# Performance work log

Hardware: AMD Instinct MI355X
Metric: run time of the kernel (lower is better)

The kernel has to match this reference:

```python
import jax, jax.numpy as jnp
import numpy as np
import math

H = 4          # n_heads
LAM = 2.0      # gate_lambda
EPS = 1e-6


def _evid_gate(t, W, b):
    # t: [B,T,d] -> g: [B,T,1] via Normal-Inverse-Gamma evidential gate
    h = t @ W.T + b                                  # [B,T,4]
    mu, v_raw, a_raw, b_raw = jnp.split(h, 4, axis=-1)
    v = jax.nn.softplus(v_raw) + EPS
    alpha = jax.nn.softplus(a_raw) + 1.0 + EPS
    beta = jax.nn.softplus(b_raw) + EPS
    var_ep = beta / (v * (alpha - 1.0))
    g = jax.nn.sigmoid(mu) * jnp.exp(-LAM * var_ep)
    return jnp.maximum(g, 1e-6)


def _ln(t, g, b):
    m = jnp.mean(t, axis=-1, keepdims=True)
    v = jnp.var(t, axis=-1, keepdims=True)
    return (t - m) / jnp.sqrt(v + 1e-5) * g + b


def _split(t):
    B, T, d = t.shape
    return t.reshape(B, T, H, d // H).transpose(0, 2, 1, 3)  # [B,H,T,dk]


def _merge(t):
    B, h, T, dk = t.shape
    return t.transpose(0, 2, 1, 3).reshape(B, T, h * dk)


def _gated_attn(q, k, v, lg_q, lg_k, mask_k, dk):
    # q:[B,H,Tq,dk], k/v:[B,H,Tk,dk], lg_q:[B,Tq], lg_k:[B,Tk], mask_k:[B,Tk] bool
    s = jnp.einsum('bhqd,bhkd->bhqk', q, k) / math.sqrt(dk)
    s = s + lg_q[:, None, :, None] + lg_k[:, None, None, :]
    s = jnp.where(mask_k[:, None, None, :], s, -jnp.inf)
    a = jax.nn.softmax(s, axis=-1)                   # dropout is identity in eval
    return jnp.einsum('bhqk,bhkd->bhqd', a, v)


def setup_inputs():
    key = jax.random.key(0)
    ks = jax.random.split(key, 20)
    B, Nx, Ny, d = 16, 512, 1024, 256
    s = 0.02
    w = lambda k, shape: jax.random.normal(k, shape, jnp.float32) * s
    return {
        'x': jax.random.normal(ks[0], (B, Nx, d), jnp.float32),
        'y': jax.random.normal(ks[1], (B, Ny, d), jnp.float32),
        'x_mask': jnp.ones((B, Nx), bool),
        'y_mask': jnp.ones((B, Ny), bool),
        'Wqx': w(ks[2], (d, d)), 'Wkx': w(ks[3], (d, d)), 'Wvx': w(ks[4], (d, d)),
        'Wqy': w(ks[5], (d, d)), 'Wky': w(ks[6], (d, d)), 'Wvy': w(ks[7], (d, d)),
        'gWx': w(ks[8], (4, d)), 'gbx': jnp.zeros((4,), jnp.float32),
        'gWy': w(ks[9], (4, d)), 'gby': jnp.zeros((4,), jnp.float32),
        'Wox': w(ks[10], (d, d)), 'Woy': w(ks[11], (d, d)),
        'lnx_g': jnp.ones((d,), jnp.float32), 'lnx_b': jnp.zeros((d,), jnp.float32),
        'lny_g': jnp.ones((d,), jnp.float32), 'lny_b': jnp.zeros((d,), jnp.float32),
        'ffx_W': w(ks[12], (d, d)), 'ffx_b': jnp.zeros((d,), jnp.float32),
        'ffy_W': w(ks[13], (d, d)), 'ffy_b': jnp.zeros((d,), jnp.float32),
    }


def reference(x, y, x_mask, y_mask, Wqx, Wkx, Wvx, Wqy, Wky, Wvy,
              gWx, gbx, gWy, gby, Wox, Woy,
              lnx_g, lnx_b, lny_g, lny_b, ffx_W, ffx_b, ffy_W, ffy_b):
    d = x.shape[-1]
    dk = d // H
    qx, kx, vx = _split(x @ Wqx.T), _split(x @ Wkx.T), _split(x @ Wvx.T)
    qy, ky, vy = _split(y @ Wqy.T), _split(y @ Wky.T), _split(y @ Wvy.T)
    gx = _evid_gate(x, gWx, gbx)                     # [B,Nx,1]
    gy = _evid_gate(y, gWy, gby)                     # [B,Ny,1]
    lgx = jnp.log(gx)[..., 0]                        # [B,Nx]
    lgy = jnp.log(gy)[..., 0]                        # [B,Ny]

    out_x = _merge(_gated_attn(qx, ky, vy, lgx, lgy, y_mask, dk)) @ Wox.T
    x2 = _ln(x + out_x, lnx_g, lnx_b)
    x2 = _ln(x2 + jax.nn.silu(x2 @ ffx_W.T + ffx_b), lnx_g, lnx_b)

    out_y = _merge(_gated_attn(qy, kx, vx, lgy, lgx, x_mask, dk)) @ Woy.T
    y2 = _ln(y + out_y, lny_g, lny_b)
    y2 = _ln(y2 + jax.nn.silu(y2 @ ffy_W.T + ffy_b), lny_g, lny_b)

    return x2, y2, gx[..., 0], gy[..., 0]
```

## Files before the change

### kernel.cpp

```cpp
#include <hip/hip_runtime.h>
#include <stdint.h>

typedef unsigned short u16;
typedef unsigned int   u32;
typedef __attribute__((ext_vector_type(8))) short bf16x8;
typedef __attribute__((ext_vector_type(4))) float f32x4;

__device__ __forceinline__ u16 f2b(float f) {
    union { float f; u32 i; } v; v.f = f;
    return (u16)((v.i + 0x7fffu + ((v.i >> 16) & 1u)) >> 16);
}
__device__ __forceinline__ float b2f(u16 u) {
    union { float f; u32 i; } v; v.i = ((u32)u) << 16; return v.f;
}
__device__ __forceinline__ bf16x8 pack8(const float* s) {
    union { bf16x8 v; u16 u[8]; } r;
    #pragma unroll
    for (int i = 0; i < 8; i++) r.u[i] = f2b(s[i]);
    return r.v;
}
__device__ __forceinline__ float softplus_f(float x) {
    return x > 15.f ? x : log1pf(__expf(x));
}

__global__ __launch_bounds__(256) void prep(
    const float* __restrict__ X, const float* __restrict__ Y,
    const float* __restrict__ gWx, const float* __restrict__ gbx,
    const float* __restrict__ gWy, const float* __restrict__ gby,
    float* __restrict__ goutx, float* __restrict__ lgx,
    float* __restrict__ gouty, float* __restrict__ lgy,
    u16* __restrict__ xb, u16* __restrict__ yb,
    const float* p0, const float* p1, const float* p2, const float* p3,
    const float* p4, const float* p5, const float* p6, const float* p7,
    const float* p8, const float* p9, u16* __restrict__ wdst)
{
    const int blk = blockIdx.x;
    const int t = threadIdx.x;
    if (blk < 6144) {
        int tok = blk * 4 + (t >> 6);
        const int lane = t & 63;
        const bool isx = tok < 8192;
        const float* T  = isx ? X : Y;
        const float* gW = isx ? gWx : gWy;
        const float* gb = isx ? gbx : gby;
        float* go = isx ? goutx : gouty;
        float* lg = isx ? lgx : lgy;
        if (!isx) tok -= 8192;
        const float* xp = T + (size_t)tok * 256;
        float a0 = 0.f, a1 = 0.f, a2 = 0.f, a3 = 0.f;
        #pragma unroll
        for (int i = 0; i < 4; i++) {
            int c = lane + i * 64;
            float xv = xp[c];
            a0 += xv * gW[0 * 256 + c];
            a1 += xv * gW[1 * 256 + c];
            a2 += xv * gW[2 * 256 + c];
            a3 += xv * gW[3 * 256 + c];
        }
        #pragma unroll
        for (int off = 32; off > 0; off >>= 1) {
            a0 += __shfl_xor(a0, off);
            a1 += __shfl_xor(a1, off);
            a2 += __shfl_xor(a2, off);
            a3 += __shfl_xor(a3, off);
        }
        if (lane == 0) {
            float mu    = a0 + gb[0];
            float v     = softplus_f(a1 + gb[1]) + 1e-6f;
            float alpha = softplus_f(a2 + gb[2]) + 1.0f + 1e-6f;
            float beta  = softplus_f(a3 + gb[3]) + 1e-6f;
            float var_ep = beta / (v * (alpha - 1.0f));
            float sig = 1.0f / (1.0f + __expf(-mu));
            float g = fmaxf(sig * __expf(-2.0f * var_ep), 1e-6f);
            go[tok] = g;
            lg[tok] = logf(g);
        }
    } else if (blk < 9216) {
        int g = (blk - 6144) * 256 + t;
        const float* src; u16* dst; size_t off;
        if (g < 262144) { src = X; dst = xb; off = (size_t)g * 8; }
        else            { src = Y; dst = yb; off = (size_t)(g - 262144) * 8; }
        float tmp[8];
        *(float4*)&tmp[0] = *(const float4*)(src + off);
        *(float4*)&tmp[4] = *(const float4*)(src + off + 4);
        *(bf16x8*)(dst + off) = pack8(tmp);
    } else {
        int g = (blk - 9216) * 256 + t;
        int wsel = g >> 13, off = g & 8191;
        const float* src;
        switch (wsel) {
            case 0: src = p0; break; case 1: src = p1; break;
            case 2: src = p2; break; case 3: src = p3; break;
            case 4: src = p4; break; case 5: src = p5; break;
            case 6: src = p6; break; case 7: src = p7; break;
            case 8: src = p8; break; default: src = p9; break;
        }
        float tmp[8];
        *(float4*)&tmp[0] = *(const float4*)(src + (size_t)off * 8);
        *(float4*)&tmp[4] = *(const float4*)(src + (size_t)off * 8 + 4);
        *(bf16x8*)(wdst + ((size_t)wsel * 65536) + (size_t)off * 8) = pack8(tmp);
    }
}

__global__ __launch_bounds__(256, 2) void gemm_qkv(
    const u16* __restrict__ Axb, const u16* __restrict__ Ayb,
    const u16* __restrict__ Wx, const u16* __restrict__ Wy,
    u16* __restrict__ Qx, u16* __restrict__ Kx, u16* __restrict__ VTx,
    u16* __restrict__ Qy, u16* __restrict__ Ky, u16* __restrict__ VTy)
{
    __shared__ short smem[2 * 128 * 72];
    short* As = smem;
    short* Ws = smem + 128 * 72;
    const int t = threadIdx.x;
    const int bn = blockIdx.x;
    int bm = blockIdx.y;
    const bool isx = bm < 64;
    const u16* A  = isx ? Axb : Ayb;
    const u16* W  = isx ? Wx : Wy;
    u16* Qo  = isx ? Qx : Qy;
    u16* Ko  = isx ? Kx : Ky;
    u16* VTo = isx ? VTx : VTy;
    const int tqsh = isx ? 9 : 10;
    if (!isx) bm -= 64;

    const int w = t >> 6, lane = t & 63, li = lane & 15, quad = lane >> 4;
    const int wm = (w >> 1) * 64, wn = (w & 1) * 64;
    const int sr = t >> 1, scb = (t & 1) * 32;

    f32x4 zero = {0.f, 0.f, 0.f, 0.f};
    f32x4 acc[4][4];
    #pragma unroll
    for (int a = 0; a < 4; a++)
        #pragma unroll
        for (int b = 0; b < 4; b++) acc[a][b] = zero;

    for (int ch = 0; ch < 4; ch++) {
        const int k0 = ch * 64;
        if (ch) __syncthreads();
        {
            const u16* Ap = A + (size_t)(bm * 128 + sr) * 256 + k0 + scb;
            const u16* Wp = W + (size_t)(bn * 128 + sr) * 256 + k0 + scb;
            #pragma unroll
            for (int j = 0; j < 4; j++) {
                *(uint4*)&As[sr * 72 + scb + j * 8] = *(const uint4*)(Ap + j * 8);
                *(uint4*)&Ws[sr * 72 + scb + j * 8] = *(const uint4*)(Wp + j * 8);
            }
        }
        __syncthreads();
        #pragma unroll
        for (int c = 0; c < 2; c++) {
            bf16x8 af[4], bf[4];
            #pragma unroll
            for (int mt = 0; mt < 4; mt++)
                af[mt] = *(const bf16x8*)&As[(wm + mt * 16 + li) * 72 + c * 32 + quad * 8];
            #pragma unroll
            for (int nt = 0; nt < 4; nt++)
                bf[nt] = *(const bf16x8*)&Ws[(wn + nt * 16 + li) * 72 + c * 32 + quad * 8];
            #pragma unroll
            for (int mt = 0; mt < 4; mt++)
                #pragma unroll
                for (int nt = 0; nt < 4; nt++)
                    acc[mt][nt] = __builtin_amdgcn_mfma_f32_16x16x32_bf16(
                        af[mt], bf[nt], acc[mt][nt], 0, 0, 0);
        }
    }

    const int sel = bn >> 1;
    if (sel < 2) {
        u16* Co = (sel == 0) ? Qo : Ko;
        #pragma unroll
        for (int nt = 0; nt < 4; nt++) {
            const int c = (bn * 128 + wn + nt * 16 + li) & 255;
            #pragma unroll
            for (int mt = 0; mt < 4; mt++) {
                const int row0 = bm * 128 + wm + mt * 16 + quad * 4;
                #pragma unroll
                for (int i = 0; i < 4; i++)
                    Co[(size_t)(row0 + i) * 256 + c] = f2b(acc[mt][nt][i]);
            }
        }
    } else {
        __syncthreads();
        short* Trans = smem;
        #pragma unroll
        for (int nt = 0; nt < 4; nt++) {
            const int cl = wn + nt * 16 + li;
            #pragma unroll
            for (int mt = 0; mt < 4; mt++) {
                const int rl0 = wm + mt * 16 + quad * 4;
                #pragma unroll
                for (int i = 0; i < 4; i++)
                    Trans[cl * 136 + rl0 + i] = (short)f2b(acc[mt][nt][i]);
            }
        }
        __syncthreads();
        const int dl = t >> 1, seg = t & 1;
        const int col = (bn - 4) * 128 + dl;
        const int h = col >> 6, dd = col & 63;
        const int bz = (bm * 128) >> tqsh;
        const int key0 = (bm * 128) & ((1 << tqsh) - 1);
        u16* dst = VTo + ((((size_t)(bz * 4 + h)) * 64 + dd) << tqsh) + key0 + seg * 64;
        #pragma unroll
        for (int k = 0; k < 8; k++)
            *(uint4*)(dst + k * 8) = *(const uint4*)&Trans[dl * 136 + seg * 64 + k * 8];
    }
}

__global__ __launch_bounds__(256, 3) void attn3(
    const u16* __restrict__ Q1, const u16* __restrict__ K1, const u16* __restrict__ VT1,
    const float* __restrict__ LG1, u16* __restrict__ O1,
    const u16* __restrict__ Q2, const u16* __restrict__ K2, const u16* __restrict__ VT2,
    const float* __restrict__ LG2, u16* __restrict__ O2)
{
    __shared__ short Ks[64][72];
    __shared__ short VTs[64][72];
    __shared__ short Ps[128][72];
    __shared__ float Lk[64];

    const int t = threadIdx.x;
    const int h = blockIdx.y, bz = blockIdx.z;
    const bool ph1 = blockIdx.x < 4;
    const int qtl = ph1 ? blockIdx.x : blockIdx.x - 4;
    const u16* Q  = ph1 ? Q1 : Q2;
    const u16* K  = ph1 ? K1 : K2;
    const u16* VT = ph1 ? VT1 : VT2;
    const float* LG = ph1 ? LG1 : LG2;
    u16* O = ph1 ? O1 : O2;
    const int Tq = ph1 ? 512 : 1024;
    const int Tk = ph1 ? 1024 : 512;

    const int w = t >> 6, lane = t & 63, li = lane & 15, quad = lane >> 4;
    const int q0 = qtl * 128;

    bf16x8 qf[2][2];
    #pragma unroll
    for (int s = 0; s < 2; s++) {
        const u16* qp = Q + (size_t)(bz * Tq + q0 + s * 64 + w * 16 + li) * 256 + h * 64 + quad * 8;
        qf[s][0] = *(const bf16x8*)qp;
        qf[s][1] = *(const bf16x8*)(qp + 32);
    }

    float lsum[2] = {0.f, 0.f};
    f32x4 zero = {0.f, 0.f, 0.f, 0.f};
    f32x4 oacc[2][4];
    #pragma unroll
    for (int s = 0; s < 2; s++)
        #pragma unroll
        for (int md = 0; md < 4; md++) oacc[s][md] = zero;

    const int sr = t >> 2, sc = (t & 3) * 16;
    const u16* Kp  = K + (size_t)(bz * Tk + sr) * 256 + h * 64 + sc;
    const u16* VTp = VT + ((size_t)(bz * 4 + h) * 64 + sr) * Tk + sc;
    const float* LGp = LG + (size_t)bz * Tk;

    uint4 pk0, pk1, pv0, pv1;
    float plk;
    pk0 = *(const uint4*)(Kp);
    pk1 = *(const uint4*)(Kp + 8);
    pv0 = *(const uint4*)(VTp);
    pv1 = *(const uint4*)(VTp + 8);
    plk = (t < 64) ? LGp[t] : 0.f;

    for (int kt = 0; kt < Tk; kt += 64) {
        __syncthreads();
        *(uint4*)&Ks[sr][sc]      = pk0;
        *(uint4*)&Ks[sr][sc + 8]  = pk1;
        *(uint4*)&VTs[sr][sc]     = pv0;
        *(uint4*)&VTs[sr][sc + 8] = pv1;
        if (t < 64) Lk[t] = plk;
        __syncthreads();
        if (kt + 64 < Tk) {
            pk0 = *(const uint4*)(Kp + (size_t)(kt + 64) * 256);
            pk1 = *(const uint4*)(Kp + (size_t)(kt + 64) * 256 + 8);
            pv0 = *(const uint4*)(VTp + kt + 64);
            pv1 = *(const uint4*)(VTp + kt + 64 + 8);
            if (t < 64) plk = LGp[kt + 64 + t];
        }

        #pragma unroll
        for (int s = 0; s < 2; s++) {
            f32x4 sacc[4] = {zero, zero, zero, zero};
            #pragma unroll
            for (int c = 0; c < 2; c++)
                #pragma unroll
                for (int mt = 0; mt < 4; mt++) {
                    bf16x8 af = *(const bf16x8*)&Ks[mt * 16 + li][c * 32 + quad * 8];
                    sacc[mt] = __builtin_amdgcn_mfma_f32_16x16x32_bf16(af, qf[s][c], sacc[mt], 0, 0, 0);
                }
            #pragma unroll
            for (int mt = 0; mt < 4; mt++) {
                float4 lk4 = *(const float4*)&Lk[mt * 16 + quad * 4];
                float p0 = __expf(sacc[mt][0] * 0.125f + lk4.x);
                float p1 = __expf(sacc[mt][1] * 0.125f + lk4.y);
                float p2 = __expf(sacc[mt][2] * 0.125f + lk4.z);
                float p3 = __expf(sacc[mt][3] * 0.125f + lk4.w);
                lsum[s] += (p0 + p1) + (p2 + p3);
                uint2 st;
                st.x = (u32)f2b(p0) | ((u32)f2b(p1) << 16);
                st.y = (u32)f2b(p2) | ((u32)f2b(p3) << 16);
                *(uint2*)&Ps[s * 64 + w * 16 + li][mt * 16 + quad * 4] = st;
            }
        }

        #pragma unroll
        for (int c = 0; c < 2; c++) {
            bf16x8 vf[4], pf[2];
            #pragma unroll
            for (int md = 0; md < 4; md++)
                vf[md] = *(const bf16x8*)&VTs[md * 16 + li][c * 32 + quad * 8];
            #pragma unroll
            for (int s = 0; s < 2; s++)
                pf[s] = *(const bf16x8*)&Ps[s * 64 + w * 16 + li][c * 32 + quad * 8];
            #pragma unroll
            for (int s = 0; s < 2; s++)
                #pragma unroll
                for (int md = 0; md < 4; md++)
                    oacc[s][md] = __builtin_amdgcn_mfma_f32_16x16x32_bf16(
                        vf[md], pf[s], oacc[s][md], 0, 0, 0);
        }
    }

    #pragma unroll
    for (int s = 0; s < 2; s++) {
        float l = lsum[s];
        l += __shfl_xor(l, 16);
        l += __shfl_xor(l, 32);
        const float inv = 1.0f / l;
        u16* op = O + (size_t)(bz * Tq + q0 + s * 64 + w * 16 + li) * 256 + h * 64;
        #pragma unroll
        for (int md = 0; md < 4; md++)
            #pragma unroll
            for (int i = 0; i < 4; i++)
                op[md * 16 + quad * 4 + i] = f2b(oacc[s][md][i] * inv);
    }
}

template<int ACT>
__global__ __launch_bounds__(256, 2) void gemm_ln(
    const u16* __restrict__ Axb, const u16* __restrict__ Ayb,
    const u16* __restrict__ Wxb, const u16* __restrict__ Wyb,
    const float* __restrict__ bx, const float* __restrict__ by,
    const float* __restrict__ Rx, const float* __restrict__ Ry,
    const float* __restrict__ gxv, const float* __restrict__ bxv,
    const float* __restrict__ gyv, const float* __restrict__ byv,
    float* __restrict__ Fx, float* __restrict__ Fy,
    u16* __restrict__ Bx, u16* __restrict__ By)
{
    __shared__ short As[64 * 72];
    __shared__ short Ws[256 * 72];
    __shared__ float Sred[64][4];
    __shared__ float Ssq[64][4];

    const int t = threadIdx.x;
    int blk = blockIdx.x;
    const bool isx = blk < 128;
    const u16* A = isx ? Axb : Ayb;
    const u16* W = isx ? Wxb : Wyb;
    const float* bias  = isx ? bx : by;
    const float* RES   = isx ? Rx : Ry;
    const float* gamma = isx ? gxv : gyv;
    const float* beta  = isx ? bxv : byv;
    float* F = isx ? Fx : Fy;
    u16*   B = isx ? Bx : By;
    if (!isx) blk -= 128;
    const int r0 = blk * 64;

    const int w = t >> 6, lane = t & 63, li = lane & 15, quad = lane >> 4;
    const int wn = w * 64;

    f32x4 zero = {0.f, 0.f, 0.f, 0.f};
    f32x4 acc[4][4];
    #pragma unroll
    for (int a = 0; a < 4; a++)
        #pragma unroll
        for (int b = 0; b < 4; b++) acc[a][b] = zero;

    const int asr = t >> 2, asc = (t & 3) * 16;
    const int wr0 = t >> 3, wseg = (t & 7) * 8;
    for (int ch = 0; ch < 4; ch++) {
        const int k0 = ch * 64;
        if (ch) __syncthreads();
        {
            const u16* Ap = A + (size_t)(r0 + asr) * 256 + k0 + asc;
            *(uint4*)&As[asr * 72 + asc]     = *(const uint4*)Ap;
            *(uint4*)&As[asr * 72 + asc + 8] = *(const uint4*)(Ap + 8);
            #pragma unroll
            for (int jj = 0; jj < 8; jj++) {
                const int row = wr0 + jj * 32;
                *(uint4*)&Ws[row * 72 + wseg] =
                    *(const uint4*)(W + (size_t)row * 256 + k0 + wseg);
            }
        }
        __syncthreads();
        #pragma unroll
        for (int c = 0; c < 2; c++) {
            bf16x8 af[4], bf[4];
            #pragma unroll
            for (int mt = 0; mt < 4; mt++)
                af[mt] = *(const bf16x8*)&As[(mt * 16 + li) * 72 + c * 32 + quad * 8];
            #pragma unroll
            for (int nt = 0; nt < 4; nt++)
                bf[nt] = *(const bf16x8*)&Ws[(wn + nt * 16 + li) * 72 + c * 32 + quad * 8];
            #pragma unroll
            for (int mt = 0; mt < 4; mt++)
                #pragma unroll
                for (int nt = 0; nt < 4; nt++)
                    acc[mt][nt] = __builtin_amdgcn_mfma_f32_16x16x32_bf16(
                        af[mt], bf[nt], acc[mt][nt], 0, 0, 0);
        }
    }

    float bv[4], gv[4], btv[4];
    #pragma unroll
    for (int nt = 0; nt < 4; nt++) {
        const int col = wn + nt * 16 + li;
        bv[nt]  = bias ? bias[col] : 0.f;
        gv[nt]  = gamma[col];
        btv[nt] = beta[col];
    }
    float psum[4][4], psq[4][4];
    #pragma unroll
    for (int mt = 0; mt < 4; mt++) {
        #pragma unroll
        for (int i = 0; i < 4; i++) { psum[mt][i] = 0.f; psq[mt][i] = 0.f; }
        #pragma unroll
        for (int nt = 0; nt < 4; nt++) {
            const int col = wn + nt * 16 + li;
            #pragma unroll
            for (int i = 0; i < 4; i++) {
                float v = acc[mt][nt][i] + bv[nt];
                if (ACT) v = v / (1.f + __expf(-v));
                const int row = mt * 16 + quad * 4 + i;
                v += RES[(size_t)(r0 + row) * 256 + col];
                acc[mt][nt][i] = v;
                psum[mt][i] += v;
                psq[mt][i]  += v * v;
            }
        }
        #pragma unroll
        for (int i = 0; i < 4; i++) {
            #pragma unroll
            for (int off = 1; off < 16; off <<= 1) {
                psum[mt][i] += __shfl_xor(psum[mt][i], off);
                psq[mt][i]  += __shfl_xor(psq[mt][i], off);
            }
        }
    }
    if (li == 0) {
        #pragma unroll
        for (int mt = 0; mt < 4; mt++)
            #pragma unroll
            for (int i = 0; i < 4; i++) {
                Sred[mt * 16 + quad * 4 + i][w] = psum[mt][i];
                Ssq[mt * 16 + quad * 4 + i][w]  = psq[mt][i];
            }
    }
    __syncthreads();
    #pragma unroll
    for (int mt = 0; mt < 4; mt++) {
        #pragma unroll
        for (int i = 0; i < 4; i++) {
            const int row = mt * 16 + quad * 4 + i;
            float4 s4 = *(const float4*)&Sred[row][0];
            float4 q4 = *(const float4*)&Ssq[row][0];
            float S  = (s4.x + s4.y) + (s4.z + s4.w);
            float S2 = (q4.x + q4.y) + (q4.z + q4.w);
            float mean = S * (1.0f / 256.0f);
            float var  = S2 * (1.0f / 256.0f) - mean * mean;
            float rstd = rsqrtf(var + 1e-5f);
            #pragma unroll
            for (int nt = 0; nt < 4; nt++) {
                const int col = wn + nt * 16 + li;
                float outv = (acc[mt][nt][i] - mean) * rstd * gv[nt] + btv[nt];
                F[(size_t)(r0 + row) * 256 + col] = outv;
                if (B) B[(size_t)(r0 + row) * 256 + col] = f2b(outv);
            }
        }
    }
}

extern "C" void kernel_launch(void* const* d_in, const int* in_sizes, int n_in,
                              void* d_out, int out_size, void* d_ws, size_t ws_size,
                              hipStream_t stream)
{
    const float* x = (const float*)d_in[0];
    const float* y = (const float*)d_in[1];
    const int wb = (n_in >= 24) ? 4 : 2;
    const float* Wqx  = (const float*)d_in[wb + 0];
    const float* Wkx  = (const float*)d_in[wb + 1];
    const float* Wvx  = (const float*)d_in[wb + 2];
    const float* Wqy  = (const float*)d_in[wb + 3];
    const float* Wky  = (const float*)d_in[wb + 4];
    const float* Wvy  = (const float*)d_in[wb + 5];
    const float* gWx  = (const float*)d_in[wb + 6];
    const float* gbx  = (const float*)d_in[wb + 7];
    const float* gWy  = (const float*)d_in[wb + 8];
    const float* gby  = (const float*)d_in[wb + 9];
    const float* Wox  = (const float*)d_in[wb + 10];
    const float* Woy  = (const float*)d_in[wb + 11];
    const float* lnxg = (const float*)d_in[wb + 12];
    const float* lnxb = (const float*)d_in[wb + 13];
    const float* lnyg = (const float*)d_in[wb + 14];
    const float* lnyb = (const float*)d_in[wb + 15];
    const float* ffxW = (const float*)d_in[wb + 16];
    const float* ffxb = (const float*)d_in[wb + 17];
    const float* ffyW = (const float*)d_in[wb + 18];
    const float* ffyb = (const float*)d_in[wb + 19];

    char* ws = (char*)d_ws;
    float* lgx = (float*)(ws);
    float* lgy = (float*)(ws + 32768);
    u16* wbf   = (u16*)(ws + 98304);
    u16* xbf   = (u16*)(ws + 1409024);
    u16* ybf   = xbf + (size_t)8192 * 256;
    u16* qb    = ybf + (size_t)16384 * 256;
    u16* kb    = qb  + (size_t)8192 * 256;
    u16* vtb   = kb  + (size_t)16384 * 256;
    u16* qb2   = vtb + (size_t)16384 * 256;
    u16* kb2   = qb2 + (size_t)16384 * 256;
    u16* vtb2  = kb2 + (size_t)8192 * 256;
    u16* ctxx  = vtb2 + (size_t)8192 * 256;
    u16* ctxy  = ctxx + (size_t)8192 * 256;
    u16* xa    = ctxy + (size_t)16384 * 256;
    u16* ya    = xa + (size_t)8192 * 256;

    float* out_x2 = (float*)d_out;
    float* out_y2 = out_x2 + 2097152;
    float* out_gx = out_x2 + 6291456;
    float* out_gy = out_x2 + 6299648;

    prep<<<9536, 256, 0, stream>>>(
        x, y, gWx, gbx, gWy, gby, out_gx, lgx, out_gy, lgy,
        xbf, ybf,
        Wqx, Wkx, Wvx, Wqy, Wky, Wvy, Wox, Woy, ffxW, ffyW, wbf);
    gemm_qkv<<<dim3(6, 192), 256, 0, stream>>>(
        xbf, ybf, wbf + 0 * 65536, wbf + 3 * 65536,
        qb, kb2, vtb2, qb2, kb, vtb);
    attn3<<<dim3(12, 4, 16), 256, 0, stream>>>(
        qb, kb, vtb, lgy, ctxx, qb2, kb2, vtb2, lgx, ctxy);
    gemm_ln<0><<<384, 256, 0, stream>>>(
        ctxx, ctxy, wbf + 6 * 65536, wbf + 7 * 65536,
        nullptr, nullptr, x, y,
        lnxg, lnxb, lnyg, lnyb, out_x2, out_y2, xa, ya);
    gemm_ln<1><<<384, 256, 0, stream>>>(
        xa, ya, wbf + 8 * 65536, wbf + 9 * 65536,
        ffxb, ffyb, out_x2, out_y2,
        lnxg, lnxb, lnyg, lnyb, out_x2, out_y2, nullptr, nullptr);

    (void)in_sizes; (void)out_size; (void)ws_size;
}
```

Measured before the change: 234.5 us.

## Double-buffer attention K/V tiles, use exp2 with hardware bf16 packing, halve LN-GEMM row tile

The attention kernel now double-buffers the K, V^T and log-gate tiles in shared memory, which drops one barrier per iteration. It interleaves the P·V MFMA per query sub-tile, so the P scratch buffer shrinks to 64 rows. Softmax uses v_exp_f32 with the scale folded into log2 units, and the gate logits are stored as log2. bf16 packing uses v_cvt_pk_bf16_f32 instead of software rounding. Separately, the fused GEMM+LayerNorm kernels switch to 32-row tiles with twice as many blocks and higher occupancy bounds, trading more weight-tile reloads for better parallelism.

```diff
diff --git a/kernel.cpp b/kernel.cpp
--- a/kernel.cpp
+++ b/kernel.cpp
@@ -73,7 +73,7 @@
             float sig = 1.0f / (1.0f + __expf(-mu));
             float g = fmaxf(sig * __expf(-2.0f * var_ep), 1e-6f);
             go[tok] = g;
-            lg[tok] = logf(g);
+            lg[tok] = log2f(g);
         }
     } else if (blk < 9216) {
         int g = (blk - 6144) * 256 + t;
@@ -212,10 +212,10 @@
     const u16* __restrict__ Q2, const u16* __restrict__ K2, const u16* __restrict__ VT2,
     const float* __restrict__ LG2, u16* __restrict__ O2)
 {
-    __shared__ short Ks[64][72];
-    __shared__ short VTs[64][72];
-    __shared__ short Ps[128][72];
-    __shared__ float Lk[64];
+    __shared__ short Ks[2][64][72];
+    __shared__ short VTs[2][64][72];
+    __shared__ short Ps[64][72];
+    __shared__ float Lk[2][64];
 
     const int t = threadIdx.x;
     const int h = blockIdx.y, bz = blockIdx.z;
@@ -253,21 +253,21 @@
     const u16* VTp = VT + ((size_t)(bz * 4 + h) * 64 + sr) * Tk + sc;
     const float* LGp = LG + (size_t)bz * Tk;
 
-    uint4 pk0, pk1, pv0, pv1;
-    float plk;
-    pk0 = *(const uint4*)(Kp);
-    pk1 = *(const uint4*)(Kp + 8);
-    pv0 = *(const uint4*)(VTp);
-    pv1 = *(const uint4*)(VTp + 8);
-    plk = (t < 64) ? LGp[t] : 0.f;
-
+    uint4 pk0 = *(const uint4*)(Kp);
+    uint4 pk1 = *(const uint4*)(Kp + 8);
+    uint4 pv0 = *(const uint4*)(VTp);
+    uint4 pv1 = *(const uint4*)(VTp + 8);
+    float plk = (t < 64) ? LGp[t] : 0.f;
+
+    const float SCL = 0.18033688f;
+
+    int cur = 0;
     for (int kt = 0; kt < Tk; kt += 64) {
-        __syncthreads();
-        *(uint4*)&Ks[sr][sc]      = pk0;
-        *(uint4*)&Ks[sr][sc + 8]  = pk1;
-        *(uint4*)&VTs[sr][sc]     = pv0;
-        *(uint4*)&VTs[sr][sc + 8] = pv1;
-        if (t < 64) Lk[t] = plk;
+        *(uint4*)&Ks[cur][sr][sc]       = pk0;
+        *(uint4*)&Ks[cur][sr][sc + 8]   = pk1;
+        *(uint4*)&VTs[cur][sr][sc]      = pv0;
+        *(uint4*)&VTs[cur][sr][sc + 8]  = pv1;
+        if (t < 64) Lk[cur][t] = plk;
         __syncthreads();
         if (kt + 64 < Tk) {
             pk0 = *(const uint4*)(Kp + (size_t)(kt + 64) * 256);
@@ -277,6 +277,13 @@
             if (t < 64) plk = LGp[kt + 64 + t];
         }
 
+        bf16x8 vf[2][4];
+        #pragma unroll
+        for (int c = 0; c < 2; c++)
+            #pragma unroll
+            for (int md = 0; md < 4; md++)
+                vf[c][md] = *(const bf16x8*)&VTs[cur][md * 16 + li][c * 32 + quad * 8];
+
         #pragma unroll
         for (int s = 0; s < 2; s++) {
             f32x4 sacc[4] = {zero, zero, zero, zero};
@@ -284,40 +291,38 @@
             for (int c = 0; c < 2; c++)
                 #pragma unroll
                 for (int mt = 0; mt < 4; mt++) {
-                    bf16x8 af = *(const bf16x8*)&Ks[mt * 16 + li][c * 32 + quad * 8];
+                    bf16x8 af = *(const bf16x8*)&Ks[cur][mt * 16 + li][c * 32 + quad * 8];
                     sacc[mt] = __builtin_amdgcn_mfma_f32_16x16x32_bf16(af, qf[s][c], sacc[mt], 0, 0, 0);
                 }
             #pragma unroll
             for (int mt = 0; mt < 4; mt++) {
-                float4 lk4 = *(const float4*)&Lk[mt * 16 + quad * 4];
-                float p0 = __expf(sacc[mt][0] * 0.125f + lk4.x);
-                float p1 = __expf(sacc[mt][1] * 0.125f + lk4.y);
-                float p2 = __expf(sacc[mt][2] * 0.125f + lk4.z);
-                float p3 = __expf(sacc[mt][3] * 0.125f + lk4.w);
+                float4 lk4 = *(const float4*)&Lk[cur][mt * 16 + quad * 4];
+                float x0 = fmaf(sacc[mt][0], SCL, lk4.x);
+                float x1 = fmaf(sacc[mt][1], SCL, lk4.y);
+                float x2 = fmaf(sacc[mt][2], SCL, lk4.z);
+                float x3 = fmaf(sacc[mt][3], SCL, lk4.w);
+                float p0, p1, p2, p3;
+                asm("v_exp_f32 %0, %1" : "=v"(p0) : "v"(x0));
+                asm("v_exp_f32 %0, %1" : "=v"(p1) : "v"(x1));
+                asm("v_exp_f32 %0, %1" : "=v"(p2) : "v"(x2));
+                asm("v_exp_f32 %0, %1" : "=v"(p3) : "v"(x3));
                 lsum[s] += (p0 + p1) + (p2 + p3);
-                uint2 st;
-                st.x = (u32)f2b(p0) | ((u32)f2b(p1) << 16);
-                st.y = (u32)f2b(p2) | ((u32)f2b(p3) << 16);
-                *(uint2*)&Ps[s * 64 + w * 16 + li][mt * 16 + quad * 4] = st;
-            }
-        }
-
-        #pragma unroll
-        for (int c = 0; c < 2; c++) {
-            bf16x8 vf[4], pf[2];
-            #pragma unroll
-            for (int md = 0; md < 4; md++)
-                vf[md] = *(const bf16x8*)&VTs[md * 16 + li][c * 32 + quad * 8];
-            #pragma unroll
-            for (int s = 0; s < 2; s++)
-                pf[s] = *(const bf16x8*)&Ps[s * 64 + w * 16 + li][c * 32 + quad * 8];
-            #pragma unroll
-            for (int s = 0; s < 2; s++)
+                u32 lo, hi;
+                asm("v_cvt_pk_bf16_f32 %0, %1, %2" : "=v"(lo) : "v"(p0), "v"(p1));
+                asm("v_cvt_pk_bf16_f32 %0, %1, %2" : "=v"(hi) : "v"(p2), "v"(p3));
+                uint2 st; st.x = lo; st.y = hi;
+                *(uint2*)&Ps[w * 16 + li][mt * 16 + quad * 4] = st;
+            }
+            #pragma unroll
+            for (int c = 0; c < 2; c++) {
+                bf16x8 pfv = *(const bf16x8*)&Ps[w * 16 + li][c * 32 + quad * 8];
                 #pragma unroll
                 for (int md = 0; md < 4; md++)
                     oacc[s][md] = __builtin_amdgcn_mfma_f32_16x16x32_bf16(
-                        vf[md], pf[s], oacc[s][md], 0, 0, 0);
-        }
+                        vf[c][md], pfv, oacc[s][md], 0, 0, 0);
+            }
+        }
+        cur ^= 1;
     }
 
     #pragma unroll
@@ -328,15 +333,22 @@
         const float inv = 1.0f / l;
         u16* op = O + (size_t)(bz * Tq + q0 + s * 64 + w * 16 + li) * 256 + h * 64;
         #pragma unroll
-        for (int md = 0; md < 4; md++)
-            #pragma unroll
-            for (int i = 0; i < 4; i++)
-                op[md * 16 + quad * 4 + i] = f2b(oacc[s][md][i] * inv);
+        for (int md = 0; md < 4; md++) {
+            float o0 = oacc[s][md][0] * inv;
+            float o1 = oacc[s][md][1] * inv;
+            float o2 = oacc[s][md][2] * inv;
+            float o3 = oacc[s][md][3] * inv;
+            u32 lo, hi;
+            asm("v_cvt_pk_bf16_f32 %0, %1, %2" : "=v"(lo) : "v"(o0), "v"(o1));
+            asm("v_cvt_pk_bf16_f32 %0, %1, %2" : "=v"(hi) : "v"(o2), "v"(o3));
+            uint2 st; st.x = lo; st.y = hi;
+            *(uint2*)(op + md * 16 + quad * 4) = st;
+        }
     }
 }
 
 template<int ACT>
-__global__ __launch_bounds__(256, 2) void gemm_ln(
+__global__ __launch_bounds__(256, 3) void gemm_ln(
     const u16* __restrict__ Axb, const u16* __restrict__ Ayb,
     const u16* __restrict__ Wxb, const u16* __restrict__ Wyb,
     const float* __restrict__ bx, const float* __restrict__ by,
@@ -346,14 +358,14 @@
     float* __restrict__ Fx, float* __restrict__ Fy,
     u16* __restrict__ Bx, u16* __restrict__ By)
 {
-    __shared__ short As[64 * 72];
+    __shared__ short As[32 * 72];
     __shared__ short Ws[256 * 72];
-    __shared__ float Sred[64][4];
-    __shared__ float Ssq[64][4];
+    __shared__ float Sred[32][4];
+    __shared__ float Ssq[32][4];
 
     const int t = threadIdx.x;
     int blk = blockIdx.x;
-    const bool isx = blk < 128;
+    const bool isx = blk < 256;
     const u16* A = isx ? Axb : Ayb;
     const u16* W = isx ? Wxb : Wyb;
     const float* bias  = isx ? bx : by;
@@ -362,28 +374,27 @@
     const float* beta  = isx ? bxv : byv;
     float* F = isx ? Fx : Fy;
     u16*   B = isx ? Bx : By;
-    if (!isx) blk -= 128;
-    const int r0 = blk * 64;
+    if (!isx) blk -= 256;
+    const int r0 = blk * 32;
 
     const int w = t >> 6, lane = t & 63, li = lane & 15, quad = lane >> 4;
     const int wn = w * 64;
 
     f32x4 zero = {0.f, 0.f, 0.f, 0.f};
-    f32x4 acc[4][4];
-    #pragma unroll
-    for (int a = 0; a < 4; a++)
+    f32x4 acc[2][4];
+    #pragma unroll
+    for (int a = 0; a < 2; a++)
         #pragma unroll
         for (int b = 0; b < 4; b++) acc[a][b] = zero;
 
-    const int asr = t >> 2, asc = (t & 3) * 16;
+    const int asr = t >> 3, asc = (t & 7) * 8;
     const int wr0 = t >> 3, wseg = (t & 7) * 8;
     for (int ch = 0; ch < 4; ch++) {
         const int k0 = ch * 64;
         if (ch) __syncthreads();
         {
-            const u16* Ap = A + (size_t)(r0 + asr) * 256 + k0 + asc;
-            *(uint4*)&As[asr * 72 + asc]     = *(const uint4*)Ap;
-            *(uint4*)&As[asr * 72 + asc + 8] = *(const uint4*)(Ap + 8);
+            *(uint4*)&As[asr * 72 + asc] =
+                *(const uint4*)(A + (size_t)(r0 + asr) * 256 + k0 + asc);
             #pragma unroll
             for (int jj = 0; jj < 8; jj++) {
                 const int row = wr0 + jj * 32;
@@ -394,15 +405,15 @@
         __syncthreads();
         #pragma unroll
         for (int c = 0; c < 2; c++) {
-            bf16x8 af[4], bf[4];
-            #pragma unroll
-            for (int mt = 0; mt < 4; mt++)
+            bf16x8 af[2], bf[4];
+            #pragma unroll
+            for (int mt = 0; mt < 2; mt++)
                 af[mt] = *(const bf16x8*)&As[(mt * 16 + li) * 72 + c * 32 + quad * 8];
             #pragma unroll
             for (int nt = 0; nt < 4; nt++)
                 bf[nt] = *(const bf16x8*)&Ws[(wn + nt * 16 + li) * 72 + c * 32 + quad * 8];
             #pragma unroll
-            for (int mt = 0; mt < 4; mt++)
+            for (int mt = 0; mt < 2; mt++)
                 #pragma unroll
                 for (int nt = 0; nt < 4; nt++)
                     acc[mt][nt] = __builtin_amdgcn_mfma_f32_16x16x32_bf16(
@@ -418,9 +429,9 @@
         gv[nt]  = gamma[col];
         btv[nt] = beta[col];
     }
-    float psum[4][4], psq[4][4];
-    #pragma unroll
-    for (int mt = 0; mt < 4; mt++) {
+    float psum[2][4], psq[2][4];
+    #pragma unroll
+    for (int mt = 0; mt < 2; mt++) {
         #pragma unroll
         for (int i = 0; i < 4; i++) { psum[mt][i] = 0.f; psq[mt][i] = 0.f; }
         #pragma unroll
@@ -448,7 +459,7 @@
     }
     if (li == 0) {
         #pragma unroll
-        for (int mt = 0; mt < 4; mt++)
+        for (int mt = 0; mt < 2; mt++)
             #pragma unroll
             for (int i = 0; i < 4; i++) {
                 Sred[mt * 16 + quad * 4 + i][w] = psum[mt][i];
@@ -457,7 +468,7 @@
     }
     __syncthreads();
     #pragma unroll
-    for (int mt = 0; mt < 4; mt++) {
+    for (int mt = 0; mt < 2; mt++) {
         #pragma unroll
         for (int i = 0; i < 4; i++) {
             const int row = mt * 16 + quad * 4 + i;
@@ -538,11 +549,11 @@
         qb, kb2, vtb2, qb2, kb, vtb);
     attn3<<<dim3(12, 4, 16), 256, 0, stream>>>(
         qb, kb, vtb, lgy, ctxx, qb2, kb2, vtb2, lgx, ctxy);
-    gemm_ln<0><<<384, 256, 0, stream>>>(
+    gemm_ln<0><<<768, 256, 0, stream>>>(
         ctxx, ctxy, wbf + 6 * 65536, wbf + 7 * 65536,
         nullptr, nullptr, x, y,
         lnxg, lnxb, lnyg, lnyb, out_x2, out_y2, xa, ya);
-    gemm_ln<1><<<384, 256, 0, stream>>>(
+    gemm_ln<1><<<768, 256, 0, stream>>>(
         xa, ya, wbf + 8 * 65536, wbf + 9 * 65536,
         ffxb, ffyb, out_x2, out_y2,
         lnxg, lnxb, lnyg, lnyb, out_x2, out_y2, nullptr, nullptr);
```

Result: slower. 253.2 us (+7.9%).
